# Kernel optimization log

Measured on AMD Instinct MI355X. Metric: run time of the kernel, lower is better.

The kernel has to match this reference:

```python
import jax, jax.numpy as jnp
import numpy as np

B, N, D, H, DG = 1, 1024, 512, 8, 64
DK = D // H
EPS = 1e-5


def _layer_norm(x, g, b):
    m = jnp.mean(x, axis=-1, keepdims=True)
    v = jnp.var(x, axis=-1, keepdims=True)
    return (x - m) / jnp.sqrt(v + EPS) * g + b


def _box_rel_embedding(box):
    # box: (B, N, 4) = x_min, y_min, x_max, y_max
    x_min, y_min, x_max, y_max = [box[..., i] for i in range(4)]  # each (B, N)
    cx = (x_min + x_max) * 0.5
    cy = (y_min + y_max) * 0.5
    w = x_max - x_min + 1.0
    h = y_max - y_min + 1.0
    dx = jnp.log(jnp.clip(jnp.abs((cx[:, :, None] - cx[:, None, :]) / w[:, :, None]), 0.001))
    dy = jnp.log(jnp.clip(jnp.abs((cy[:, :, None] - cy[:, None, :]) / h[:, :, None]), 0.001))
    dw = jnp.log(w[:, :, None] / w[:, None, :])
    dh = jnp.log(h[:, :, None] / h[:, None, :])
    pos = jnp.stack([dx, dy, dw, dh], axis=-1)  # (B, N, N, 4)
    dim_mat = 1.0 / jnp.power(1000.0, jnp.arange(DG // 8, dtype=jnp.float32) / (DG // 8))  # (8,)
    mul = (100.0 * pos[..., None] * dim_mat).reshape(pos.shape[0], pos.shape[1], pos.shape[2], -1)  # (B,N,N,32)
    return jnp.concatenate([jnp.sin(mul), jnp.cos(mul)], axis=-1)  # (B, N, N, 64)


def _split_heads(x, W, b):
    # torch permute(2,0,1,3).view(-1, len, d_k): head-major flattening
    return (x @ W.T + b).reshape(B, N, H, DK).transpose(2, 0, 1, 3).reshape(H * B, N, DK)


def _forward(input_query, input_key, input_value, input_box,
             Wq, bq, Wk, bk, Wv, bv, Wo, bo, WG_w, WG_b,
             ln0_g, ln0_b, ln_g, ln_b):
    residual = input_query
    emb = _box_rel_embedding(input_box)  # (B, N, N, 64)
    # per-head linear (64 -> 1) then relu: (B, H, N, N)
    w_g = jax.nn.relu(jnp.einsum('bijg,hg->bhij', emb, WG_w) + WG_b[None, :, None, None])
    q = _split_heads(input_query, Wq, bq)  # (H*B, N, DK)
    k = _split_heads(input_key, Wk, bk)
    v = _split_heads(input_value, Wv, bv)
    scores = jnp.einsum('xnd,xmd->xnm', q, k) / np.sqrt(DK).astype(np.float32)  # (H*B, N, N)
    # original adds (B,H,N,N) to (H*B,N,N): only valid for B==1
    w_mn = jax.nn.softmax(jnp.log(jnp.clip(w_g.reshape(H * B, N, N), 1e-6)) + scores, axis=-1)
    x = jnp.einsum('xnm,xmd->xnd', w_mn, v)  # (H*B, N, DK)
    # faithful to original: transpose(1,2) then view(nbatches, -1, h*d_k)
    x = x.transpose(0, 2, 1).reshape(B, -1, H * DK)  # (B, N, D)
    out0 = _layer_norm(x + residual, ln0_g, ln0_b)
    out = out0 @ Wo.T + bo  # dropout = identity (eval mode)
    return _layer_norm(out + out0, ln_g, ln_b)


def setup_inputs() -> dict:
    key = jax.random.key(0)
    ks = jax.random.split(key, 12)
    inp = {}
    inp['input_query'] = jax.random.normal(ks[0], (B, N, D), dtype=jnp.float32)
    inp['input_key'] = jax.random.normal(ks[1], (B, N, D), dtype=jnp.float32)
    inp['input_value'] = jax.random.normal(ks[2], (B, N, D), dtype=jnp.float32)
    mins = jax.random.uniform(ks[3], (B, N, 2), dtype=jnp.float32) * 500.0
    sizes = jax.random.uniform(ks[4], (B, N, 2), dtype=jnp.float32) * 99.0 + 1.0
    inp['input_box'] = jnp.concatenate([mins, mins + sizes], axis=-1)  # valid boxes
    s = 0.02
    inp['Wq'] = jax.random.normal(ks[5], (D, D), dtype=jnp.float32) * s
    inp['bq'] = jnp.zeros((D,), dtype=jnp.float32)
    inp['Wk'] = jax.random.normal(ks[6], (D, D), dtype=jnp.float32) * s
    inp['bk'] = jnp.zeros((D,), dtype=jnp.float32)
    inp['Wv'] = jax.random.normal(ks[7], (D, D), dtype=jnp.float32) * s
    inp['bv'] = jnp.zeros((D,), dtype=jnp.float32)
    inp['Wo'] = jax.random.normal(ks[8], (D, D), dtype=jnp.float32) * s
    inp['bo'] = jnp.zeros((D,), dtype=jnp.float32)
    inp['WG_w'] = jax.random.normal(ks[9], (H, DG), dtype=jnp.float32) * 0.1
    inp['WG_b'] = jax.random.normal(ks[10], (H,), dtype=jnp.float32) * 0.1
    inp['ln0_g'] = jnp.ones((D,), dtype=jnp.float32)
    inp['ln0_b'] = jnp.zeros((D,), dtype=jnp.float32)
    inp['ln_g'] = jnp.ones((D,), dtype=jnp.float32)
    inp['ln_b'] = jnp.zeros((D,), dtype=jnp.float32)
    return inp


def reference(input_query, input_key, input_value, input_box,
              Wq, bq, Wk, bk, Wv, bv, Wo, bo, WG_w, WG_b,
              ln0_g, ln0_b, ln_g, ln_b):
    return _forward(input_query, input_key, input_value, input_box,
                    Wq, bq, Wk, bk, Wv, bv, Wo, bo, WG_w, WG_b,
                    ln0_g, ln0_b, ln_g, ln_b)
```

## Files before the change

### kernel.cpp

```cpp
#include <hip/hip_runtime.h>
#include <cstddef>

#define NTOK 1024
#define DMODEL 512
#define NHEAD 8
#define DKH 64
#define NSPLIT 4
#define JQ 256

typedef __attribute__((ext_vector_type(4))) float f32x4;
typedef __attribute__((ext_vector_type(8))) __bf16 bf16x8;
typedef __attribute__((ext_vector_type(4))) __bf16 bf16x4;
typedef __attribute__((ext_vector_type(4))) unsigned short u16x4;
typedef __attribute__((ext_vector_type(8))) unsigned short u16x8;
typedef __attribute__((ext_vector_type(4))) _Float16 f16x4;
typedef unsigned short ushort_t;

__device__ __forceinline__ float wave_sum_f(float v){
  #pragma unroll
  for (int m=1; m<64; m<<=1) v += __shfl_xor(v, m, 64);
  return v;
}
__device__ __forceinline__ unsigned short f2bf(float f){
  __bf16 b = (__bf16)f;
  return __builtin_bit_cast(unsigned short, b);
}
__device__ __forceinline__ float bf2f(unsigned short u){
  return (float)__builtin_bit_cast(__bf16, u);
}

__device__ __forceinline__ float fract_hw(float x){
  float r; asm("v_fract_f32 %0, %1" : "=v"(r) : "v"(x)); return r;
}
__device__ __forceinline__ float sin_rev(float rev){
  float f = fract_hw(rev);
  float s; asm("v_sin_f32 %0, %1" : "=v"(s) : "v"(f)); return s;
}
__device__ __forceinline__ float cos_rev(float rev){
  float f = fract_hw(rev);
  float c; asm("v_cos_f32 %0, %1" : "=v"(c) : "v"(f)); return c;
}
__device__ __forceinline__ float log_hw(float x){
  float l; asm("v_log_f32 %0, %1" : "=v"(l) : "v"(x));
  return 0.69314718056f * l;
}
__device__ __forceinline__ float exp_hw(float x){
  float y = x * 1.44269504f;
  float e; asm("v_exp_f32 %0, %1" : "=v"(e) : "v"(y));
  return e;
}

__global__ __launch_bounds__(256) void k_pre(
    const float* __restrict__ box, const float* __restrict__ WGw, const float* __restrict__ WGb,
    _Float16* __restrict__ wg16,
    const float* __restrict__ q, const float* __restrict__ k, const float* __restrict__ v,
    const float* __restrict__ wq, const float* __restrict__ wk, const float* __restrict__ wv,
    const float* __restrict__ wo,
    ushort_t* __restrict__ qb, ushort_t* __restrict__ kb, ushort_t* __restrict__ vb,
    ushort_t* __restrict__ wqb, ushort_t* __restrict__ wkb, ushort_t* __restrict__ wvb,
    ushort_t* __restrict__ wob){
  const int t = threadIdx.x;
  if (blockIdx.x >= 1024){
    int gi = (blockIdx.x - 1024)*256 + t;
    const float* s; ushort_t* d; int off;
    if (gi < 196608){
      int seg = gi >> 16;
      off = (gi & 65535)*8;
      s = seg==0 ? q : seg==1 ? k : v;
      d = seg==0 ? qb : seg==1 ? kb : vb;
    } else {
      int g2 = gi - 196608;
      int seg = g2 >> 15;
      off = (g2 & 32767)*8;
      s = seg==0 ? wq : seg==1 ? wk : seg==2 ? wv : wo;
      d = seg==0 ? wqb : seg==1 ? wkb : seg==2 ? wvb : wob;
    }
    float4 a = *(const float4*)(s + off);
    float4 b = *(const float4*)(s + off + 4);
    u16x4 o0, o1;
    o0[0]=f2bf(a.x); o0[1]=f2bf(a.y); o0[2]=f2bf(a.z); o0[3]=f2bf(a.w);
    o1[0]=f2bf(b.x); o1[1]=f2bf(b.y); o1[2]=f2bf(b.z); o1[3]=f2bf(b.w);
    *(u16x4*)(d + off) = o0;
    *(u16x4*)(d + off + 4) = o1;
    return;
  }
  __shared__ float arr[4][1024];
  #pragma unroll
  for (int u=0; u<4; u++){
    int idx = u*256 + t;
    float4 b4 = *(const float4*)(box + idx*4);
    arr[0][idx] = (b4.x + b4.z)*0.5f;
    arr[1][idx] = (b4.y + b4.w)*0.5f;
    arr[2][idx] = log_hw(b4.z - b4.x + 1.0f);
    arr[3][idx] = log_hw(b4.w - b4.y + 1.0f);
  }
  const int i = blockIdx.x;
  const int lane = t & 63, w = t >> 6, li = lane & 15, g = lane >> 4;
  float4 bi = *(const float4*)(box + i*4);
  float wi = bi.z - bi.x + 1.0f, hi = bi.w - bi.y + 1.0f;
  float Pi = (g==0) ? (bi.x+bi.z)*0.5f : (g==1) ? (bi.y+bi.w)*0.5f
           : (g==2) ? log_hw(wi) : log_hw(hi);
  float Ri = (g==0) ? 1.0f/wi : (g==1) ? 1.0f/hi : 1.0f;
  const bool doLog = (g < 2);
  bf16x8 wfs = {}, wfc = {};
  float wgb_li = 0.0f;
  if (li < 8){
    #pragma unroll
    for (int e=0; e<8; e++){
      wfs[e] = (__bf16)WGw[li*64 + g*8 + e];
      wfc[e] = (__bf16)WGw[li*64 + 32 + g*8 + e];
    }
    wgb_li = WGb[li];
  }
  __syncthreads();
  const float* parr = &arr[g][0];
  const float DMrev[8] = {15.9154943f, 6.7115094f, 2.8302196f, 1.1934938f,
                          0.5032921f, 0.2122365f, 0.08949941f, 0.0377416f};
  const int jbeg = w*256;
  for (int it=0; it<16; ++it){
    int j = jbeg + it*16 + li;
    float diff = (Pi - parr[j])*Ri;
    float lg = log_hw(fmaxf(fabsf(diff), 1e-3f));
    float dv = doLog ? lg : diff;
    bf16x8 afs, afc;
    #pragma unroll
    for (int e=0; e<8; e++){
      float rev = dv * DMrev[e];
      afs[e] = (__bf16)sin_rev(rev);
      afc[e] = (__bf16)cos_rev(rev);
    }
    f32x4 acc = (f32x4){0.f,0.f,0.f,0.f};
    acc = __builtin_amdgcn_mfma_f32_16x16x32_bf16(afs, wfs, acc, 0,0,0);
    acc = __builtin_amdgcn_mfma_f32_16x16x32_bf16(afc, wfc, acc, 0,0,0);
    if (li < 8){
      f16x4 o;
      #pragma unroll
      for (int r=0; r<4; r++)
        o[r] = (_Float16)fmaxf(acc[r] + wgb_li, 6.103515625e-05f);
      *(f16x4*)(wg16 + (((size_t)li<<20) + ((size_t)i<<10) + jbeg + it*16 + g*4)) = o;
    }
  }
}

__global__ __launch_bounds__(128) void k_mm_qkv(
    const ushort_t* __restrict__ Aq, const ushort_t* __restrict__ Ak, const ushort_t* __restrict__ Av,
    const ushort_t* __restrict__ Wqb, const ushort_t* __restrict__ Wkb, const ushort_t* __restrict__ Wvb,
    const float* __restrict__ bq, const float* __restrict__ bk, const float* __restrict__ bv,
    ushort_t* __restrict__ Qb, ushort_t* __restrict__ Kb, ushort_t* __restrict__ Vt){
  const int z = blockIdx.z;
  const ushort_t* A = z==0 ? Aq : z==1 ? Ak : Av;
  const ushort_t* W = z==0 ? Wqb : z==1 ? Wkb : Wvb;
  const float* bias = z==0 ? bq : z==1 ? bk : bv;
  const int t = threadIdx.x, lane = t & 63, w = t >> 6;
  const int li = lane & 15, g = lane >> 4;
  const int m0 = blockIdx.y*32;
  const int n0 = blockIdx.x*64 + w*32;
  const ushort_t* ar = A + (size_t)(m0+li)*DMODEL + g*8;
  const ushort_t* wr = W + (size_t)(n0+li)*DMODEL + g*8;
  f32x4 acc[2][2] = {};
  if (z < 2){
    #pragma unroll
    for (int k0=0; k0<DMODEL; k0+=64){
      bf16x8 wf0a = *(const bf16x8*)(wr + k0);
      bf16x8 wf0b = *(const bf16x8*)(wr + k0 + 32);
      bf16x8 wf1a = *(const bf16x8*)(wr + 16*DMODEL + k0);
      bf16x8 wf1b = *(const bf16x8*)(wr + 16*DMODEL + k0 + 32);
      bf16x8 af0a = *(const bf16x8*)(ar + k0);
      bf16x8 af0b = *(const bf16x8*)(ar + k0 + 32);
      bf16x8 af1a = *(const bf16x8*)(ar + 16*DMODEL + k0);
      bf16x8 af1b = *(const bf16x8*)(ar + 16*DMODEL + k0 + 32);
      acc[0][0] = __builtin_amdgcn_mfma_f32_16x16x32_bf16(wf0a, af0a, acc[0][0], 0,0,0);
      acc[0][0] = __builtin_amdgcn_mfma_f32_16x16x32_bf16(wf0b, af0b, acc[0][0], 0,0,0);
      acc[0][1] = __builtin_amdgcn_mfma_f32_16x16x32_bf16(wf0a, af1a, acc[0][1], 0,0,0);
      acc[0][1] = __builtin_amdgcn_mfma_f32_16x16x32_bf16(wf0b, af1b, acc[0][1], 0,0,0);
      acc[1][0] = __builtin_amdgcn_mfma_f32_16x16x32_bf16(wf1a, af0a, acc[1][0], 0,0,0);
      acc[1][0] = __builtin_amdgcn_mfma_f32_16x16x32_bf16(wf1b, af0b, acc[1][0], 0,0,0);
      acc[1][1] = __builtin_amdgcn_mfma_f32_16x16x32_bf16(wf1a, af1a, acc[1][1], 0,0,0);
      acc[1][1] = __builtin_amdgcn_mfma_f32_16x16x32_bf16(wf1b, af1b, acc[1][1], 0,0,0);
    }
    ushort_t* C = z ? Kb : Qb;
    #pragma unroll
    for (int nf=0; nf<2; nf++){
      int n = n0 + nf*16 + g*4;
      float4 b4 = *(const float4*)(bias + n);
      const float* bp = (const float*)&b4;
      #pragma unroll
      for (int mf=0; mf<2; mf++){
        int m = m0 + mf*16 + li;
        u16x4 o;
        #pragma unroll
        for (int r=0; r<4; r++) o[r] = f2bf(acc[nf][mf][r] + bp[r]);
        *(u16x4*)(C + (size_t)m*DMODEL + n) = o;
      }
    }
  } else {
    #pragma unroll
    for (int k0=0; k0<DMODEL; k0+=64){
      bf16x8 wf0a = *(const bf16x8*)(wr + k0);
      bf16x8 wf0b = *(const bf16x8*)(wr + k0 + 32);
      bf16x8 wf1a = *(const bf16x8*)(wr + 16*DMODEL + k0);
      bf16x8 wf1b = *(const bf16x8*)(wr + 16*DMODEL + k0 + 32);
      bf16x8 af0a = *(const bf16x8*)(ar + k0);
      bf16x8 af0b = *(const bf16x8*)(ar + k0 + 32);
      bf16x8 af1a = *(const bf16x8*)(ar + 16*DMODEL + k0);
      bf16x8 af1b = *(const bf16x8*)(ar + 16*DMODEL + k0 + 32);
      acc[0][0] = __builtin_amdgcn_mfma_f32_16x16x32_bf16(af0a, wf0a, acc[0][0], 0,0,0);
      acc[0][0] = __builtin_amdgcn_mfma_f32_16x16x32_bf16(af0b, wf0b, acc[0][0], 0,0,0);
      acc[0][1] = __builtin_amdgcn_mfma_f32_16x16x32_bf16(af0a, wf1a, acc[0][1], 0,0,0);
      acc[0][1] = __builtin_amdgcn_mfma_f32_16x16x32_bf16(af0b, wf1b, acc[0][1], 0,0,0);
      acc[1][0] = __builtin_amdgcn_mfma_f32_16x16x32_bf16(af1a, wf0a, acc[1][0], 0,0,0);
      acc[1][0] = __builtin_amdgcn_mfma_f32_16x16x32_bf16(af1b, wf0b, acc[1][0], 0,0,0);
      acc[1][1] = __builtin_amdgcn_mfma_f32_16x16x32_bf16(af1a, wf1a, acc[1][1], 0,0,0);
      acc[1][1] = __builtin_amdgcn_mfma_f32_16x16x32_bf16(af1b, wf1b, acc[1][1], 0,0,0);
    }
    #pragma unroll
    for (int mf=0; mf<2; mf++){
      int m = m0 + mf*16 + g*4;
      #pragma unroll
      for (int nf=0; nf<2; nf++){
        int n = n0 + nf*16 + li;
        float bn = bias[n];
        u16x4 o;
        #pragma unroll
        for (int r=0; r<4; r++) o[r] = f2bf(acc[mf][nf][r] + bn);
        *(u16x4*)(Vt + (((size_t)(n>>6))<<16) + ((size_t)(n&63)<<10) + m) = o;
      }
    }
  }
}

__global__ __launch_bounds__(512) void k_attn3(const ushort_t* __restrict__ Qb,
     const ushort_t* __restrict__ Kb, const ushort_t* __restrict__ Vt,
     const _Float16* __restrict__ wg, ushort_t* __restrict__ Xpt, float* __restrict__ rsp){
  __shared__ ushort_t Ks[256*68];
  __shared__ ushort_t Vs[64*264];
  const int t = threadIdx.x;
  const int itg = blockIdx.x, h = blockIdx.y, sp = blockIdx.z;
  const int jbeg = sp*JQ;
  {
    const int r = t >> 3, c = (t & 7)*8;
    #pragma unroll
    for (int p=0; p<4; p++){
      u16x8 kv = *(const u16x8*)(Kb + (size_t)(jbeg + p*64 + r)*DMODEL + h*DKH + c);
      *(u16x8*)(Ks + (p*64 + r)*68 + c) = kv;
      u16x8 vv = *(const u16x8*)(Vt + ((size_t)h<<16) + (size_t)r*NTOK + jbeg + p*64 + c);
      *(u16x8*)(Vs + r*264 + p*64 + c) = vv;
    }
  }
  const int lane = t & 63, w = t >> 6;
  const int i0 = (itg*8 + w)*16;
  const int li = lane & 15, g = lane >> 4;
  const ushort_t* qp = Qb + (size_t)(i0+li)*DMODEL + h*DKH + g*8;
  bf16x8 qf0 = *(const bf16x8*)(qp);
  bf16x8 qf1 = *(const bf16x8*)(qp + 32);
  const _Float16* gbase = wg + ((size_t)h<<20) + ((size_t)(i0+li)<<10) + jbeg + g*4;
  f32x4 xacc[4];
  #pragma unroll
  for (int mf=0; mf<4; mf++) xacc[mf] = (f32x4){0.f,0.f,0.f,0.f};
  float rsum = 0.f;
  __syncthreads();
  #pragma unroll
  for (int jj = 0; jj < JQ; jj += 32){
    const ushort_t* kp = Ks + (jj + li)*68 + g*8;
    bf16x8 a00 = *(const bf16x8*)(kp);
    bf16x8 a01 = *(const bf16x8*)(kp + 32);
    bf16x8 a10 = *(const bf16x8*)(kp + 16*68);
    bf16x8 a11 = *(const bf16x8*)(kp + 16*68 + 32);
    f32x4 s0 = (f32x4){0.f,0.f,0.f,0.f};
    f32x4 s1 = (f32x4){0.f,0.f,0.f,0.f};
    s0 = __builtin_amdgcn_mfma_f32_16x16x32_bf16(a00, qf0, s0, 0,0,0);
    s0 = __builtin_amdgcn_mfma_f32_16x16x32_bf16(a01, qf1, s0, 0,0,0);
    s1 = __builtin_amdgcn_mfma_f32_16x16x32_bf16(a10, qf0, s1, 0,0,0);
    s1 = __builtin_amdgcn_mfma_f32_16x16x32_bf16(a11, qf1, s1, 0,0,0);
    f16x4 g0 = *(const f16x4*)(gbase + jj);
    f16x4 g1 = *(const f16x4*)(gbase + jj + 16);
    float p[8];
    #pragma unroll
    for (int r=0; r<4; r++){ p[r]   = (float)g0[r] * exp_hw(s0[r]*0.125f); rsum += p[r]; }
    #pragma unroll
    for (int r=0; r<4; r++){ p[4+r] = (float)g1[r] * exp_hw(s1[r]*0.125f); rsum += p[4+r]; }
    bf16x8 pb;
    pb[0]=(__bf16)p[0]; pb[1]=(__bf16)p[1]; pb[2]=(__bf16)p[2]; pb[3]=(__bf16)p[3];
    pb[4]=(__bf16)p[4]; pb[5]=(__bf16)p[5]; pb[6]=(__bf16)p[6]; pb[7]=(__bf16)p[7];
    #pragma unroll
    for (int mf=0; mf<4; mf++){
      const ushort_t* vp = Vs + (size_t)(li + mf*16)*264 + jj + g*4;
      bf16x4 lo = *(const bf16x4*)(vp);
      bf16x4 hi = *(const bf16x4*)(vp + 16);
      bf16x8 vf = __builtin_shufflevector(lo, hi, 0,1,2,3,4,5,6,7);
      xacc[mf] = __builtin_amdgcn_mfma_f32_16x16x32_bf16(vf, pb, xacc[mf], 0,0,0);
    }
  }
  rsum += __shfl_xor(rsum, 16, 64);
  rsum += __shfl_xor(rsum, 32, 64);
  if (lane < 16) rsp[((size_t)sp*NHEAD + h)*NTOK + i0 + li] = rsum;
  __syncthreads();
  float* xw = (float*)Ks + w*(16*68);
  #pragma unroll
  for (int mf=0; mf<4; mf++)
    *(f32x4*)&xw[li*68 + mf*16 + g*4] = xacc[mf];
  __builtin_amdgcn_s_waitcnt(0);
  float xv[16];
  #pragma unroll
  for (int r=0; r<16; r++) xv[r] = xw[r*68 + lane];
  u16x8 o0, o1;
  #pragma unroll
  for (int r=0; r<8; r++){ o0[r] = f2bf(xv[r]); o1[r] = f2bf(xv[8+r]); }
  ushort_t* xp = Xpt + (((size_t)sp*NHEAD + h)*DKH + lane)*NTOK + i0;
  *(u16x8*)(xp)     = o0;
  *(u16x8*)(xp + 8) = o1;
}

__global__ __launch_bounds__(256) void k_ln0c(const ushort_t* __restrict__ Xpt,
        const float* __restrict__ rsp, const float* __restrict__ resid,
        const float* __restrict__ g, const float* __restrict__ b,
        float* __restrict__ out0, ushort_t* __restrict__ out0b){
  const int n = blockIdx.x, t = threadIdx.x;
  const int h = n >> 7, dk = (n >> 1) & 63, mo = (n & 1)*512;
  const int i0 = mo + t, i1 = mo + t + 256;
  float s0v=0.f, s1v=0.f, r0=0.f, r1=0.f;
  #pragma unroll
  for (int sp=0; sp<NSPLIT; sp++){
    const ushort_t* base = Xpt + (((size_t)sp*NHEAD + h)*DKH + dk)*NTOK;
    s0v += bf2f(base[i0]);
    s1v += bf2f(base[i1]);
    const float* rb = rsp + ((size_t)sp*NHEAD + h)*NTOK;
    r0 += rb[i0];
    r1 += rb[i1];
  }
  float x0 = s0v/r0 + resid[(size_t)n*DMODEL + t];
  float x1 = s1v/r1 + resid[(size_t)n*DMODEL + t + 256];
  __shared__ float red[8];
  float s = wave_sum_f(x0 + x1);
  float q = wave_sum_f(x0*x0 + x1*x1);
  int wid = t >> 6, lane = t & 63;
  if (lane == 0){ red[wid] = s; red[4+wid] = q; }
  __syncthreads();
  float S = red[0]+red[1]+red[2]+red[3];
  float Q = red[4]+red[5]+red[6]+red[7];
  float mean = S * (1.0f/512.0f);
  float var = Q * (1.0f/512.0f) - mean*mean;
  float rs = rsqrtf(var + 1e-5f);
  float y0 = (x0-mean)*rs*g[t] + b[t];
  float y1 = (x1-mean)*rs*g[t+256] + b[t+256];
  out0[(size_t)n*DMODEL + t]        = y0;
  out0[(size_t)n*DMODEL + t + 256]  = y1;
  out0b[(size_t)n*DMODEL + t]       = f2bf(y0);
  out0b[(size_t)n*DMODEL + t + 256] = f2bf(y1);
}

__global__ __launch_bounds__(512) void k_mm_o_ln(
    const ushort_t* __restrict__ A, const ushort_t* __restrict__ W,
    const float* __restrict__ bo, const float* __restrict__ add,
    const float* __restrict__ lng, const float* __restrict__ lnb, float* __restrict__ out){
  const int t = threadIdx.x, lane = t & 63, w = t >> 6;
  const int li = lane & 15, g = lane >> 4;
  const int m0 = blockIdx.x*16;
  const int n0 = w*64;
  const ushort_t* ar = A + (size_t)(m0+li)*DMODEL + g*8;
  const ushort_t* wr = W + (size_t)(n0+li)*DMODEL + g*8;
  f32x4 acc[4] = {};
  #pragma unroll
  for (int k0=0; k0<DMODEL; k0+=64){
    bf16x8 afa = *(const bf16x8*)(ar + k0);
    bf16x8 afb = *(const bf16x8*)(ar + k0 + 32);
    #pragma unroll
    for (int nf=0; nf<4; nf++){
      const ushort_t* wp = wr + (size_t)nf*16*DMODEL + k0;
      bf16x8 wfa = *(const bf16x8*)(wp);
      bf16x8 wfb = *(const bf16x8*)(wp + 32);
      acc[nf] = __builtin_amdgcn_mfma_f32_16x16x32_bf16(wfa, afa, acc[nf], 0,0,0);
      acc[nf] = __builtin_amdgcn_mfma_f32_16x16x32_bf16(wfb, afb, acc[nf], 0,0,0);
    }
  }
  const int m = m0 + li;
  float s = 0.f, qq = 0.f;
  f32x4 v[4];
  #pragma unroll
  for (int nf=0; nf<4; nf++){
    int n = n0 + nf*16 + g*4;
    f32x4 b4 = *(const f32x4*)(bo + n);
    f32x4 a4 = *(const f32x4*)(add + (size_t)m*DMODEL + n);
    #pragma unroll
    for (int r=0; r<4; r++){
      float x = acc[nf][r] + b4[r] + a4[r];
      v[nf][r] = x; s += x; qq += x*x;
    }
  }
  s  += __shfl_xor(s, 16, 64);  s  += __shfl_xor(s, 32, 64);
  qq += __shfl_xor(qq, 16, 64); qq += __shfl_xor(qq, 32, 64);
  __shared__ float red[8][16][2];
  if (g == 0){ red[w][li][0] = s; red[w][li][1] = qq; }
  __syncthreads();
  float S = 0.f, Q = 0.f;
  #pragma unroll
  for (int u=0; u<8; u++){ S += red[u][li][0]; Q += red[u][li][1]; }
  float mean = S * (1.0f/512.0f);
  float var = Q * (1.0f/512.0f) - mean*mean;
  float rs = rsqrtf(var + 1e-5f);
  #pragma unroll
  for (int nf=0; nf<4; nf++){
    int n = n0 + nf*16 + g*4;
    f32x4 g4 = *(const f32x4*)(lng + n);
    f32x4 be = *(const f32x4*)(lnb + n);
    f32x4 o;
    #pragma unroll
    for (int r=0; r<4; r++) o[r] = (v[nf][r]-mean)*rs*g4[r] + be[r];
    *(f32x4*)(out + (size_t)m*DMODEL + n) = o;
  }
}

extern "C" void kernel_launch(void* const* d_in, const int* in_sizes, int n_in,
                              void* d_out, int out_size, void* d_ws, size_t ws_size,
                              hipStream_t stream){
  (void)in_sizes; (void)n_in; (void)out_size; (void)ws_size;
  const float* in_q = (const float*)d_in[0];
  const float* in_k = (const float*)d_in[1];
  const float* in_v = (const float*)d_in[2];
  const float* box  = (const float*)d_in[3];
  const float* Wq   = (const float*)d_in[4];
  const float* bq   = (const float*)d_in[5];
  const float* Wk   = (const float*)d_in[6];
  const float* bk   = (const float*)d_in[7];
  const float* Wv   = (const float*)d_in[8];
  const float* bv   = (const float*)d_in[9];
  const float* Wo   = (const float*)d_in[10];
  const float* bo   = (const float*)d_in[11];
  const float* WGw  = (const float*)d_in[12];
  const float* WGb  = (const float*)d_in[13];
  const float* ln0g = (const float*)d_in[14];
  const float* ln0b = (const float*)d_in[15];
  const float* lng  = (const float*)d_in[16];
  const float* lnb  = (const float*)d_in[17];

  float* ws = (float*)d_ws;
  ushort_t* Abq  = (ushort_t*)(ws + 0);
  ushort_t* Abk  = (ushort_t*)(ws + 262144);
  ushort_t* Abv  = (ushort_t*)(ws + 524288);
  ushort_t* Wqb  = (ushort_t*)(ws + 786432);
  ushort_t* Wkb  = (ushort_t*)(ws + 917504);
  ushort_t* Wvb  = (ushort_t*)(ws + 1048576);
  ushort_t* Wob  = (ushort_t*)(ws + 1179648);
  ushort_t* Qb   = (ushort_t*)(ws + 1310720);
  ushort_t* Kb   = (ushort_t*)(ws + 1572864);
  ushort_t* Vt   = (ushort_t*)(ws + 1835008);
  _Float16* wg16 = (_Float16*)(ws + 2097152);
  ushort_t* Xpt  = (ushort_t*)(ws + 6291456);
  float*    rsp  = ws + 8388608;
  float*    out0 = ws + 8421376;
  ushort_t* out0b= (ushort_t*)(ws + 8945664);
  float*    out  = (float*)d_out;

  k_pre<<<dim3(2304), dim3(256), 0, stream>>>(box, WGw, WGb, wg16,
            in_q, in_k, in_v, Wq, Wk, Wv, Wo,
            Abq, Abk, Abv, Wqb, Wkb, Wvb, Wob);
  k_mm_qkv<<<dim3(8,32,3), dim3(128), 0, stream>>>(Abq, Abk, Abv, Wqb, Wkb, Wvb,
            bq, bk, bv, Qb, Kb, Vt);
  k_attn3<<<dim3(8,8,4), dim3(512), 0, stream>>>(Qb, Kb, Vt, wg16, Xpt, rsp);
  k_ln0c<<<dim3(1024), dim3(256), 0, stream>>>(Xpt, rsp, in_q, ln0g, ln0b, out0, out0b);
  k_mm_o_ln<<<dim3(64), dim3(512), 0, stream>>>(out0b, Wob, bo, out0, lng, lnb, out);
}
```

Measured before the change: 77.92 us.

## Fuse QKV projection into box-embedding kernel and LN0 into output GEMM

The QKV projection now reads fp32 inputs and weights directly, converts them to bf16 in registers, and runs as extra blocks of the box-embedding kernel. This removes the separate bf16 conversion pass and one launch. The LN0 combine step is fused into the output-projection+LN kernel through shared memory, which drops the out0/out0b round trip and another launch. In exchange, the QKV blocks now read fp32 data at twice the bytes and redo the conversion per tile, and the back kernel runs only 64 blocks that also do the LN0 work.

```diff
diff --git a/kernel.cpp b/kernel.cpp
--- a/kernel.cpp
+++ b/kernel.cpp
@@ -9,6 +9,7 @@
 #define JQ 256
 
 typedef __attribute__((ext_vector_type(4))) float f32x4;
+typedef __attribute__((ext_vector_type(8))) float f32x8;
 typedef __attribute__((ext_vector_type(8))) __bf16 bf16x8;
 typedef __attribute__((ext_vector_type(4))) __bf16 bf16x4;
 typedef __attribute__((ext_vector_type(4))) unsigned short u16x4;
@@ -28,6 +29,10 @@
 __device__ __forceinline__ float bf2f(unsigned short u){
   return (float)__builtin_bit_cast(__bf16, u);
 }
+__device__ __forceinline__ bf16x8 cvt8(const float* p){
+  f32x8 v = *(const f32x8*)p;
+  return __builtin_convertvector(v, bf16x8);
+}
 
 __device__ __forceinline__ float fract_hw(float x){
   float r; asm("v_fract_f32 %0, %1" : "=v"(r) : "v"(x)); return r;
@@ -50,38 +55,112 @@
   return e;
 }
 
-__global__ __launch_bounds__(256) void k_pre(
+__global__ __launch_bounds__(256) void k_front(
     const float* __restrict__ box, const float* __restrict__ WGw, const float* __restrict__ WGb,
     _Float16* __restrict__ wg16,
-    const float* __restrict__ q, const float* __restrict__ k, const float* __restrict__ v,
-    const float* __restrict__ wq, const float* __restrict__ wk, const float* __restrict__ wv,
-    const float* __restrict__ wo,
-    ushort_t* __restrict__ qb, ushort_t* __restrict__ kb, ushort_t* __restrict__ vb,
-    ushort_t* __restrict__ wqb, ushort_t* __restrict__ wkb, ushort_t* __restrict__ wvb,
-    ushort_t* __restrict__ wob){
+    const float* __restrict__ inq, const float* __restrict__ ink, const float* __restrict__ inv,
+    const float* __restrict__ Wq, const float* __restrict__ Wk, const float* __restrict__ Wv,
+    const float* __restrict__ Wo,
+    const float* __restrict__ bq, const float* __restrict__ bk, const float* __restrict__ bv,
+    ushort_t* __restrict__ Qb, ushort_t* __restrict__ Kb, ushort_t* __restrict__ Vt,
+    ushort_t* __restrict__ Wob){
   const int t = threadIdx.x;
-  if (blockIdx.x >= 1024){
-    int gi = (blockIdx.x - 1024)*256 + t;
-    const float* s; ushort_t* d; int off;
-    if (gi < 196608){
-      int seg = gi >> 16;
-      off = (gi & 65535)*8;
-      s = seg==0 ? q : seg==1 ? k : v;
-      d = seg==0 ? qb : seg==1 ? kb : vb;
-    } else {
-      int g2 = gi - 196608;
-      int seg = g2 >> 15;
-      off = (g2 & 32767)*8;
-      s = seg==0 ? wq : seg==1 ? wk : seg==2 ? wv : wo;
-      d = seg==0 ? wqb : seg==1 ? wkb : seg==2 ? wvb : wob;
-    }
-    float4 a = *(const float4*)(s + off);
-    float4 b = *(const float4*)(s + off + 4);
+  const int lane = t & 63, w = t >> 6, li = lane & 15, g = lane >> 4;
+  if (blockIdx.x >= 1408){
+    int gi = (blockIdx.x - 1408)*256 + t;
+    int off = gi*8;
+    float4 a = *(const float4*)(Wo + off);
+    float4 b4 = *(const float4*)(Wo + off + 4);
     u16x4 o0, o1;
     o0[0]=f2bf(a.x); o0[1]=f2bf(a.y); o0[2]=f2bf(a.z); o0[3]=f2bf(a.w);
-    o1[0]=f2bf(b.x); o1[1]=f2bf(b.y); o1[2]=f2bf(b.z); o1[3]=f2bf(b.w);
-    *(u16x4*)(d + off) = o0;
-    *(u16x4*)(d + off + 4) = o1;
+    o1[0]=f2bf(b4.x); o1[1]=f2bf(b4.y); o1[2]=f2bf(b4.z); o1[3]=f2bf(b4.w);
+    *(u16x4*)(Wob + off) = o0;
+    *(u16x4*)(Wob + off + 4) = o1;
+    return;
+  }
+  if (blockIdx.x >= 1024){
+    const int unit = (blockIdx.x - 1024)*2 + (w >> 1);
+    const int z = unit >> 8;
+    const int rem = unit & 255;
+    const int my = rem >> 3;
+    const int nx = rem & 7;
+    const int m0 = my*32;
+    const int n0 = nx*64 + (w & 1)*32;
+    const float* A = z==0 ? inq : z==1 ? ink : inv;
+    const float* W = z==0 ? Wq : z==1 ? Wk : Wv;
+    const float* bias = z==0 ? bq : z==1 ? bk : bv;
+    const float* ar = A + (size_t)(m0+li)*DMODEL + g*8;
+    const float* wr = W + (size_t)(n0+li)*DMODEL + g*8;
+    f32x4 acc[2][2] = {};
+    if (z < 2){
+      #pragma unroll
+      for (int k0=0; k0<DMODEL; k0+=64){
+        bf16x8 wf0a = cvt8(wr + k0);
+        bf16x8 wf0b = cvt8(wr + k0 + 32);
+        bf16x8 wf1a = cvt8(wr + 16*DMODEL + k0);
+        bf16x8 wf1b = cvt8(wr + 16*DMODEL + k0 + 32);
+        bf16x8 af0a = cvt8(ar + k0);
+        bf16x8 af0b = cvt8(ar + k0 + 32);
+        bf16x8 af1a = cvt8(ar + 16*DMODEL + k0);
+        bf16x8 af1b = cvt8(ar + 16*DMODEL + k0 + 32);
+        acc[0][0] = __builtin_amdgcn_mfma_f32_16x16x32_bf16(wf0a, af0a, acc[0][0], 0,0,0);
+        acc[0][0] = __builtin_amdgcn_mfma_f32_16x16x32_bf16(wf0b, af0b, acc[0][0], 0,0,0);
+        acc[0][1] = __builtin_amdgcn_mfma_f32_16x16x32_bf16(wf0a, af1a, acc[0][1], 0,0,0);
+        acc[0][1] = __builtin_amdgcn_mfma_f32_16x16x32_bf16(wf0b, af1b, acc[0][1], 0,0,0);
+        acc[1][0] = __builtin_amdgcn_mfma_f32_16x16x32_bf16(wf1a, af0a, acc[1][0], 0,0,0);
+        acc[1][0] = __builtin_amdgcn_mfma_f32_16x16x32_bf16(wf1b, af0b, acc[1][0], 0,0,0);
+        acc[1][1] = __builtin_amdgcn_mfma_f32_16x16x32_bf16(wf1a, af1a, acc[1][1], 0,0,0);
+        acc[1][1] = __builtin_amdgcn_mfma_f32_16x16x32_bf16(wf1b, af1b, acc[1][1], 0,0,0);
+      }
+      ushort_t* C = z ? Kb : Qb;
+      #pragma unroll
+      for (int nf=0; nf<2; nf++){
+        int n = n0 + nf*16 + g*4;
+        float4 b4 = *(const float4*)(bias + n);
+        const float* bp = (const float*)&b4;
+        #pragma unroll
+        for (int mf=0; mf<2; mf++){
+          int m = m0 + mf*16 + li;
+          u16x4 o;
+          #pragma unroll
+          for (int r=0; r<4; r++) o[r] = f2bf(acc[nf][mf][r] + bp[r]);
+          *(u16x4*)(C + (size_t)m*DMODEL + n) = o;
+        }
+      }
+    } else {
+      #pragma unroll
+      for (int k0=0; k0<DMODEL; k0+=64){
+        bf16x8 wf0a = cvt8(wr + k0);
+        bf16x8 wf0b = cvt8(wr + k0 + 32);
+        bf16x8 wf1a = cvt8(wr + 16*DMODEL + k0);
+        bf16x8 wf1b = cvt8(wr + 16*DMODEL + k0 + 32);
+        bf16x8 af0a = cvt8(ar + k0);
+        bf16x8 af0b = cvt8(ar + k0 + 32);
+        bf16x8 af1a = cvt8(ar + 16*DMODEL + k0);
+        bf16x8 af1b = cvt8(ar + 16*DMODEL + k0 + 32);
+        acc[0][0] = __builtin_amdgcn_mfma_f32_16x16x32_bf16(af0a, wf0a, acc[0][0], 0,0,0);
+        acc[0][0] = __builtin_amdgcn_mfma_f32_16x16x32_bf16(af0b, wf0b, acc[0][0], 0,0,0);
+        acc[0][1] = __builtin_amdgcn_mfma_f32_16x16x32_bf16(af0a, wf1a, acc[0][1], 0,0,0);
+        acc[0][1] = __builtin_amdgcn_mfma_f32_16x16x32_bf16(af0b, wf1b, acc[0][1], 0,0,0);
+        acc[1][0] = __builtin_amdgcn_mfma_f32_16x16x32_bf16(af1a, wf0a, acc[1][0], 0,0,0);
+        acc[1][0] = __builtin_amdgcn_mfma_f32_16x16x32_bf16(af1b, wf0b, acc[1][0], 0,0,0);
+        acc[1][1] = __builtin_amdgcn_mfma_f32_16x16x32_bf16(af1a, wf1a, acc[1][1], 0,0,0);
+        acc[1][1] = __builtin_amdgcn_mfma_f32_16x16x32_bf16(af1b, wf1b, acc[1][1], 0,0,0);
+      }
+      #pragma unroll
+      for (int mf=0; mf<2; mf++){
+        int m = m0 + mf*16 + g*4;
+        #pragma unroll
+        for (int nf=0; nf<2; nf++){
+          int n = n0 + nf*16 + li;
+          float bn = bias[n];
+          u16x4 o;
+          #pragma unroll
+          for (int r=0; r<4; r++) o[r] = f2bf(acc[mf][nf][r] + bn);
+          *(u16x4*)(Vt + (((size_t)(n>>6))<<16) + ((size_t)(n&63)<<10) + m) = o;
+        }
+      }
+    }
     return;
   }
   __shared__ float arr[4][1024];
@@ -95,7 +174,6 @@
     arr[3][idx] = log_hw(b4.w - b4.y + 1.0f);
   }
   const int i = blockIdx.x;
-  const int lane = t & 63, w = t >> 6, li = lane & 15, g = lane >> 4;
   float4 bi = *(const float4*)(box + i*4);
   float wi = bi.z - bi.x + 1.0f, hi = bi.w - bi.y + 1.0f;
   float Pi = (g==0) ? (bi.x+bi.z)*0.5f : (g==1) ? (bi.y+bi.w)*0.5f
@@ -138,93 +216,6 @@
       for (int r=0; r<4; r++)
         o[r] = (_Float16)fmaxf(acc[r] + wgb_li, 6.103515625e-05f);
       *(f16x4*)(wg16 + (((size_t)li<<20) + ((size_t)i<<10) + jbeg + it*16 + g*4)) = o;
-    }
-  }
-}
-
-__global__ __launch_bounds__(128) void k_mm_qkv(
-    const ushort_t* __restrict__ Aq, const ushort_t* __restrict__ Ak, const ushort_t* __restrict__ Av,
-    const ushort_t* __restrict__ Wqb, const ushort_t* __restrict__ Wkb, const ushort_t* __restrict__ Wvb,
-    const float* __restrict__ bq, const float* __restrict__ bk, const float* __restrict__ bv,
-    ushort_t* __restrict__ Qb, ushort_t* __restrict__ Kb, ushort_t* __restrict__ Vt){
-  const int z = blockIdx.z;
-  const ushort_t* A = z==0 ? Aq : z==1 ? Ak : Av;
-  const ushort_t* W = z==0 ? Wqb : z==1 ? Wkb : Wvb;
-  const float* bias = z==0 ? bq : z==1 ? bk : bv;
-  const int t = threadIdx.x, lane = t & 63, w = t >> 6;
-  const int li = lane & 15, g = lane >> 4;
-  const int m0 = blockIdx.y*32;
-  const int n0 = blockIdx.x*64 + w*32;
-  const ushort_t* ar = A + (size_t)(m0+li)*DMODEL + g*8;
-  const ushort_t* wr = W + (size_t)(n0+li)*DMODEL + g*8;
-  f32x4 acc[2][2] = {};
-  if (z < 2){
-    #pragma unroll
-    for (int k0=0; k0<DMODEL; k0+=64){
-      bf16x8 wf0a = *(const bf16x8*)(wr + k0);
-      bf16x8 wf0b = *(const bf16x8*)(wr + k0 + 32);
-      bf16x8 wf1a = *(const bf16x8*)(wr + 16*DMODEL + k0);
-      bf16x8 wf1b = *(const bf16x8*)(wr + 16*DMODEL + k0 + 32);
-      bf16x8 af0a = *(const bf16x8*)(ar + k0);
-      bf16x8 af0b = *(const bf16x8*)(ar + k0 + 32);
-      bf16x8 af1a = *(const bf16x8*)(ar + 16*DMODEL + k0);
-      bf16x8 af1b = *(const bf16x8*)(ar + 16*DMODEL + k0 + 32);
-      acc[0][0] = __builtin_amdgcn_mfma_f32_16x16x32_bf16(wf0a, af0a, acc[0][0], 0,0,0);
-      acc[0][0] = __builtin_amdgcn_mfma_f32_16x16x32_bf16(wf0b, af0b, acc[0][0], 0,0,0);
-      acc[0][1] = __builtin_amdgcn_mfma_f32_16x16x32_bf16(wf0a, af1a, acc[0][1], 0,0,0);
-      acc[0][1] = __builtin_amdgcn_mfma_f32_16x16x32_bf16(wf0b, af1b, acc[0][1], 0,0,0);
-      acc[1][0] = __builtin_amdgcn_mfma_f32_16x16x32_bf16(wf1a, af0a, acc[1][0], 0,0,0);
-      acc[1][0] = __builtin_amdgcn_mfma_f32_16x16x32_bf16(wf1b, af0b, acc[1][0], 0,0,0);
-      acc[1][1] = __builtin_amdgcn_mfma_f32_16x16x32_bf16(wf1a, af1a, acc[1][1], 0,0,0);
-      acc[1][1] = __builtin_amdgcn_mfma_f32_16x16x32_bf16(wf1b, af1b, acc[1][1], 0,0,0);
-    }
-    ushort_t* C = z ? Kb : Qb;
-    #pragma unroll
-    for (int nf=0; nf<2; nf++){
-      int n = n0 + nf*16 + g*4;
-      float4 b4 = *(const float4*)(bias + n);
-      const float* bp = (const float*)&b4;
-      #pragma unroll
-      for (int mf=0; mf<2; mf++){
-        int m = m0 + mf*16 + li;
-        u16x4 o;
-        #pragma unroll
-        for (int r=0; r<4; r++) o[r] = f2bf(acc[nf][mf][r] + bp[r]);
-        *(u16x4*)(C + (size_t)m*DMODEL + n) = o;
-      }
-    }
-  } else {
-    #pragma unroll
-    for (int k0=0; k0<DMODEL; k0+=64){
-      bf16x8 wf0a = *(const bf16x8*)(wr + k0);
-      bf16x8 wf0b = *(const bf16x8*)(wr + k0 + 32);
-      bf16x8 wf1a = *(const bf16x8*)(wr + 16*DMODEL + k0);
-      bf16x8 wf1b = *(const bf16x8*)(wr + 16*DMODEL + k0 + 32);
-      bf16x8 af0a = *(const bf16x8*)(ar + k0);
-      bf16x8 af0b = *(const bf16x8*)(ar + k0 + 32);
-      bf16x8 af1a = *(const bf16x8*)(ar + 16*DMODEL + k0);
-      bf16x8 af1b = *(const bf16x8*)(ar + 16*DMODEL + k0 + 32);
-      acc[0][0] = __builtin_amdgcn_mfma_f32_16x16x32_bf16(af0a, wf0a, acc[0][0], 0,0,0);
-      acc[0][0] = __builtin_amdgcn_mfma_f32_16x16x32_bf16(af0b, wf0b, acc[0][0], 0,0,0);
-      acc[0][1] = __builtin_amdgcn_mfma_f32_16x16x32_bf16(af0a, wf1a, acc[0][1], 0,0,0);
-      acc[0][1] = __builtin_amdgcn_mfma_f32_16x16x32_bf16(af0b, wf1b, acc[0][1], 0,0,0);
-      acc[1][0] = __builtin_amdgcn_mfma_f32_16x16x32_bf16(af1a, wf0a, acc[1][0], 0,0,0);
-      acc[1][0] = __builtin_amdgcn_mfma_f32_16x16x32_bf16(af1b, wf0b, acc[1][0], 0,0,0);
-      acc[1][1] = __builtin_amdgcn_mfma_f32_16x16x32_bf16(af1a, wf1a, acc[1][1], 0,0,0);
-      acc[1][1] = __builtin_amdgcn_mfma_f32_16x16x32_bf16(af1b, wf1b, acc[1][1], 0,0,0);
-    }
-    #pragma unroll
-    for (int mf=0; mf<2; mf++){
-      int m = m0 + mf*16 + g*4;
-      #pragma unroll
-      for (int nf=0; nf<2; nf++){
-        int n = n0 + nf*16 + li;
-        float bn = bias[n];
-        u16x4 o;
-        #pragma unroll
-        for (int r=0; r<4; r++) o[r] = f2bf(acc[mf][nf][r] + bn);
-        *(u16x4*)(Vt + (((size_t)(n>>6))<<16) + ((size_t)(n&63)<<10) + m) = o;
-      }
     }
   }
 }
@@ -311,54 +302,56 @@
   *(u16x8*)(xp + 8) = o1;
 }
 
-__global__ __launch_bounds__(256) void k_ln0c(const ushort_t* __restrict__ Xpt,
-        const float* __restrict__ rsp, const float* __restrict__ resid,
-        const float* __restrict__ g, const float* __restrict__ b,
-        float* __restrict__ out0, ushort_t* __restrict__ out0b){
-  const int n = blockIdx.x, t = threadIdx.x;
-  const int h = n >> 7, dk = (n >> 1) & 63, mo = (n & 1)*512;
-  const int i0 = mo + t, i1 = mo + t + 256;
-  float s0v=0.f, s1v=0.f, r0=0.f, r1=0.f;
-  #pragma unroll
-  for (int sp=0; sp<NSPLIT; sp++){
-    const ushort_t* base = Xpt + (((size_t)sp*NHEAD + h)*DKH + dk)*NTOK;
-    s0v += bf2f(base[i0]);
-    s1v += bf2f(base[i1]);
-    const float* rb = rsp + ((size_t)sp*NHEAD + h)*NTOK;
-    r0 += rb[i0];
-    r1 += rb[i1];
-  }
-  float x0 = s0v/r0 + resid[(size_t)n*DMODEL + t];
-  float x1 = s1v/r1 + resid[(size_t)n*DMODEL + t + 256];
-  __shared__ float red[8];
-  float s = wave_sum_f(x0 + x1);
-  float q = wave_sum_f(x0*x0 + x1*x1);
-  int wid = t >> 6, lane = t & 63;
-  if (lane == 0){ red[wid] = s; red[4+wid] = q; }
-  __syncthreads();
-  float S = red[0]+red[1]+red[2]+red[3];
-  float Q = red[4]+red[5]+red[6]+red[7];
-  float mean = S * (1.0f/512.0f);
-  float var = Q * (1.0f/512.0f) - mean*mean;
-  float rs = rsqrtf(var + 1e-5f);
-  float y0 = (x0-mean)*rs*g[t] + b[t];
-  float y1 = (x1-mean)*rs*g[t+256] + b[t+256];
-  out0[(size_t)n*DMODEL + t]        = y0;
-  out0[(size_t)n*DMODEL + t + 256]  = y1;
-  out0b[(size_t)n*DMODEL + t]       = f2bf(y0);
-  out0b[(size_t)n*DMODEL + t + 256] = f2bf(y1);
-}
-
-__global__ __launch_bounds__(512) void k_mm_o_ln(
-    const ushort_t* __restrict__ A, const ushort_t* __restrict__ W,
-    const float* __restrict__ bo, const float* __restrict__ add,
-    const float* __restrict__ lng, const float* __restrict__ lnb, float* __restrict__ out){
+__global__ __launch_bounds__(512) void k_back(
+    const ushort_t* __restrict__ Xpt, const float* __restrict__ rsp,
+    const float* __restrict__ inq,
+    const float* __restrict__ ln0g, const float* __restrict__ ln0b,
+    const ushort_t* __restrict__ Wob, const float* __restrict__ bo,
+    const float* __restrict__ lng, const float* __restrict__ lnb,
+    float* __restrict__ out){
+  __shared__ ushort_t Ab[16][520];
+  __shared__ float    Y[16][516];
+  __shared__ float    red[8][16][2];
   const int t = threadIdx.x, lane = t & 63, w = t >> 6;
   const int li = lane & 15, g = lane >> 4;
   const int m0 = blockIdx.x*16;
+  #pragma unroll
+  for (int rr2=0; rr2<2; rr2++){
+    const int rr = w*2 + rr2;
+    const int n = m0 + rr;
+    const int h = n >> 7, dk = (n >> 1) & 63, mo = (n & 1)*512;
+    float x[8];
+    float sum = 0.f, sq = 0.f;
+    #pragma unroll
+    for (int c=0; c<8; c++){
+      int d = c*64 + lane;
+      int i = mo + d;
+      float sv = 0.f, rv = 0.f;
+      #pragma unroll
+      for (int sp=0; sp<NSPLIT; sp++){
+        sv += bf2f(Xpt[(((size_t)sp*NHEAD + h)*DKH + dk)*NTOK + i]);
+        rv += rsp[((size_t)sp*NHEAD + h)*NTOK + i];
+      }
+      x[c] = sv/rv + inq[(size_t)n*DMODEL + d];
+      sum += x[c]; sq += x[c]*x[c];
+    }
+    sum = wave_sum_f(sum);
+    sq  = wave_sum_f(sq);
+    float mean = sum * (1.0f/512.0f);
+    float var = sq * (1.0f/512.0f) - mean*mean;
+    float rs = rsqrtf(var + 1e-5f);
+    #pragma unroll
+    for (int c=0; c<8; c++){
+      int d = c*64 + lane;
+      float y = (x[c]-mean)*rs*ln0g[d] + ln0b[d];
+      Y[rr][d] = y;
+      Ab[rr][d] = f2bf(y);
+    }
+  }
+  __syncthreads();
   const int n0 = w*64;
-  const ushort_t* ar = A + (size_t)(m0+li)*DMODEL + g*8;
-  const ushort_t* wr = W + (size_t)(n0+li)*DMODEL + g*8;
+  const ushort_t* ar = &Ab[li][g*8];
+  const ushort_t* wr = Wob + (size_t)(n0+li)*DMODEL + g*8;
   f32x4 acc[4] = {};
   #pragma unroll
   for (int k0=0; k0<DMODEL; k0+=64){
@@ -380,16 +373,14 @@
   for (int nf=0; nf<4; nf++){
     int n = n0 + nf*16 + g*4;
     f32x4 b4 = *(const f32x4*)(bo + n);
-    f32x4 a4 = *(const f32x4*)(add + (size_t)m*DMODEL + n);
     #pragma unroll
     for (int r=0; r<4; r++){
-      float x = acc[nf][r] + b4[r] + a4[r];
+      float x = acc[nf][r] + b4[r] + Y[li][n + r];
       v[nf][r] = x; s += x; qq += x*x;
     }
   }
   s  += __shfl_xor(s, 16, 64);  s  += __shfl_xor(s, 32, 64);
   qq += __shfl_xor(qq, 16, 64); qq += __shfl_xor(qq, 32, 64);
-  __shared__ float red[8][16][2];
   if (g == 0){ red[w][li][0] = s; red[w][li][1] = qq; }
   __syncthreads();
   float S = 0.f, Q = 0.f;
@@ -434,29 +425,18 @@
   const float* lnb  = (const float*)d_in[17];
 
   float* ws = (float*)d_ws;
-  ushort_t* Abq  = (ushort_t*)(ws + 0);
-  ushort_t* Abk  = (ushort_t*)(ws + 262144);
-  ushort_t* Abv  = (ushort_t*)(ws + 524288);
-  ushort_t* Wqb  = (ushort_t*)(ws + 786432);
-  ushort_t* Wkb  = (ushort_t*)(ws + 917504);
-  ushort_t* Wvb  = (ushort_t*)(ws + 1048576);
-  ushort_t* Wob  = (ushort_t*)(ws + 1179648);
-  ushort_t* Qb   = (ushort_t*)(ws + 1310720);
-  ushort_t* Kb   = (ushort_t*)(ws + 1572864);
-  ushort_t* Vt   = (ushort_t*)(ws + 1835008);
-  _Float16* wg16 = (_Float16*)(ws + 2097152);
-  ushort_t* Xpt  = (ushort_t*)(ws + 6291456);
-  float*    rsp  = ws + 8388608;
-  float*    out0 = ws + 8421376;
-  ushort_t* out0b= (ushort_t*)(ws + 8945664);
+  ushort_t* Wob  = (ushort_t*)(ws + 0);
+  ushort_t* Qb   = (ushort_t*)(ws + 131072);
+  ushort_t* Kb   = (ushort_t*)(ws + 393216);
+  ushort_t* Vt   = (ushort_t*)(ws + 655360);
+  _Float16* wg16 = (_Float16*)(ws + 917504);
+  ushort_t* Xpt  = (ushort_t*)(ws + 5111808);
+  float*    rsp  = ws + 6160384;
   float*    out  = (float*)d_out;
 
-  k_pre<<<dim3(2304), dim3(256), 0, stream>>>(box, WGw, WGb, wg16,
-            in_q, in_k, in_v, Wq, Wk, Wv, Wo,
-            Abq, Abk, Abv, Wqb, Wkb, Wvb, Wob);
-  k_mm_qkv<<<dim3(8,32,3), dim3(128), 0, stream>>>(Abq, Abk, Abv, Wqb, Wkb, Wvb,
-            bq, bk, bv, Qb, Kb, Vt);
+  k_front<<<dim3(1536), dim3(256), 0, stream>>>(box, WGw, WGb, wg16,
+            in_q, in_k, in_v, Wq, Wk, Wv, Wo, bq, bk, bv, Qb, Kb, Vt, Wob);
   k_attn3<<<dim3(8,8,4), dim3(512), 0, stream>>>(Qb, Kb, Vt, wg16, Xpt, rsp);
-  k_ln0c<<<dim3(1024), dim3(256), 0, stream>>>(Xpt, rsp, in_q, ln0g, ln0b, out0, out0b);
-  k_mm_o_ln<<<dim3(64), dim3(512), 0, stream>>>(out0b, Wob, bo, out0, lng, lnb, out);
-}
+  k_back<<<dim3(64), dim3(512), 0, stream>>>(Xpt, rsp, in_q, ln0g, ln0b,
+            Wob, bo, lng, lnb, out);
+}
```

Result: slower. 83.15 us (+6.7%).

## Split attention keys eightfold and fuse split-reduce, LN0 and output projection

Applied to the files above, without the earlier changes.

The attention kernel now splits the key dimension into 8 chunks of 128 instead of 4 of 256, doubling the block count to 512 and halving per-block shared memory for better CU occupancy. The separate split-combine/LayerNorm kernel and the output-projection+LayerNorm kernel are merged into one kernel that reduces the partial sums, normalizes rows into shared memory, and feeds the MFMA projection directly. This removes one launch and the global round trip of the intermediate fp32 and bf16 activations. In exchange the reduction reads twice as many partial buffers and the fused kernel runs only 64 blocks, so the reduce phase has limited parallelism.

```diff
diff --git a/kernel.cpp b/kernel.cpp
--- a/kernel.cpp
+++ b/kernel.cpp
@@ -5,8 +5,8 @@
 #define DMODEL 512
 #define NHEAD 8
 #define DKH 64
-#define NSPLIT 4
-#define JQ 256
+#define NSPLIT 8
+#define JQ 128
 
 typedef __attribute__((ext_vector_type(4))) float f32x4;
 typedef __attribute__((ext_vector_type(8))) __bf16 bf16x8;
@@ -229,22 +229,23 @@
   }
 }
 
-__global__ __launch_bounds__(512) void k_attn3(const ushort_t* __restrict__ Qb,
+__global__ __launch_bounds__(512) void k_attn4(const ushort_t* __restrict__ Qb,
      const ushort_t* __restrict__ Kb, const ushort_t* __restrict__ Vt,
      const _Float16* __restrict__ wg, ushort_t* __restrict__ Xpt, float* __restrict__ rsp){
-  __shared__ ushort_t Ks[256*68];
-  __shared__ ushort_t Vs[64*264];
+  __shared__ __align__(16) char smem[34816];
+  ushort_t* Ks = (ushort_t*)smem;
+  ushort_t* Vs = (ushort_t*)(smem + 17408);
   const int t = threadIdx.x;
   const int itg = blockIdx.x, h = blockIdx.y, sp = blockIdx.z;
   const int jbeg = sp*JQ;
   {
     const int r = t >> 3, c = (t & 7)*8;
     #pragma unroll
-    for (int p=0; p<4; p++){
+    for (int p=0; p<2; p++){
       u16x8 kv = *(const u16x8*)(Kb + (size_t)(jbeg + p*64 + r)*DMODEL + h*DKH + c);
       *(u16x8*)(Ks + (p*64 + r)*68 + c) = kv;
       u16x8 vv = *(const u16x8*)(Vt + ((size_t)h<<16) + (size_t)r*NTOK + jbeg + p*64 + c);
-      *(u16x8*)(Vs + r*264 + p*64 + c) = vv;
+      *(u16x8*)(Vs + r*136 + p*64 + c) = vv;
     }
   }
   const int lane = t & 63, w = t >> 6;
@@ -284,7 +285,7 @@
     pb[4]=(__bf16)p[4]; pb[5]=(__bf16)p[5]; pb[6]=(__bf16)p[6]; pb[7]=(__bf16)p[7];
     #pragma unroll
     for (int mf=0; mf<4; mf++){
-      const ushort_t* vp = Vs + (size_t)(li + mf*16)*264 + jj + g*4;
+      const ushort_t* vp = Vs + (size_t)(li + mf*16)*136 + jj + g*4;
       bf16x4 lo = *(const bf16x4*)(vp);
       bf16x4 hi = *(const bf16x4*)(vp + 16);
       bf16x8 vf = __builtin_shufflevector(lo, hi, 0,1,2,3,4,5,6,7);
@@ -295,7 +296,7 @@
   rsum += __shfl_xor(rsum, 32, 64);
   if (lane < 16) rsp[((size_t)sp*NHEAD + h)*NTOK + i0 + li] = rsum;
   __syncthreads();
-  float* xw = (float*)Ks + w*(16*68);
+  float* xw = (float*)smem + w*(16*68);
   #pragma unroll
   for (int mf=0; mf<4; mf++)
     *(f32x4*)&xw[li*68 + mf*16 + g*4] = xacc[mf];
@@ -311,54 +312,56 @@
   *(u16x8*)(xp + 8) = o1;
 }
 
-__global__ __launch_bounds__(256) void k_ln0c(const ushort_t* __restrict__ Xpt,
-        const float* __restrict__ rsp, const float* __restrict__ resid,
-        const float* __restrict__ g, const float* __restrict__ b,
-        float* __restrict__ out0, ushort_t* __restrict__ out0b){
-  const int n = blockIdx.x, t = threadIdx.x;
-  const int h = n >> 7, dk = (n >> 1) & 63, mo = (n & 1)*512;
-  const int i0 = mo + t, i1 = mo + t + 256;
-  float s0v=0.f, s1v=0.f, r0=0.f, r1=0.f;
-  #pragma unroll
-  for (int sp=0; sp<NSPLIT; sp++){
-    const ushort_t* base = Xpt + (((size_t)sp*NHEAD + h)*DKH + dk)*NTOK;
-    s0v += bf2f(base[i0]);
-    s1v += bf2f(base[i1]);
-    const float* rb = rsp + ((size_t)sp*NHEAD + h)*NTOK;
-    r0 += rb[i0];
-    r1 += rb[i1];
-  }
-  float x0 = s0v/r0 + resid[(size_t)n*DMODEL + t];
-  float x1 = s1v/r1 + resid[(size_t)n*DMODEL + t + 256];
-  __shared__ float red[8];
-  float s = wave_sum_f(x0 + x1);
-  float q = wave_sum_f(x0*x0 + x1*x1);
-  int wid = t >> 6, lane = t & 63;
-  if (lane == 0){ red[wid] = s; red[4+wid] = q; }
-  __syncthreads();
-  float S = red[0]+red[1]+red[2]+red[3];
-  float Q = red[4]+red[5]+red[6]+red[7];
-  float mean = S * (1.0f/512.0f);
-  float var = Q * (1.0f/512.0f) - mean*mean;
-  float rs = rsqrtf(var + 1e-5f);
-  float y0 = (x0-mean)*rs*g[t] + b[t];
-  float y1 = (x1-mean)*rs*g[t+256] + b[t+256];
-  out0[(size_t)n*DMODEL + t]        = y0;
-  out0[(size_t)n*DMODEL + t + 256]  = y1;
-  out0b[(size_t)n*DMODEL + t]       = f2bf(y0);
-  out0b[(size_t)n*DMODEL + t + 256] = f2bf(y1);
-}
-
-__global__ __launch_bounds__(512) void k_mm_o_ln(
-    const ushort_t* __restrict__ A, const ushort_t* __restrict__ W,
-    const float* __restrict__ bo, const float* __restrict__ add,
-    const float* __restrict__ lng, const float* __restrict__ lnb, float* __restrict__ out){
+__global__ __launch_bounds__(512) void k_back(
+    const ushort_t* __restrict__ Xpt, const float* __restrict__ rsp,
+    const float* __restrict__ inq,
+    const float* __restrict__ ln0g, const float* __restrict__ ln0b,
+    const ushort_t* __restrict__ Wob, const float* __restrict__ bo,
+    const float* __restrict__ lng, const float* __restrict__ lnb,
+    float* __restrict__ out){
+  __shared__ ushort_t Ab[16][520];
+  __shared__ float    Y[16][516];
+  __shared__ float    red[8][16][2];
   const int t = threadIdx.x, lane = t & 63, w = t >> 6;
   const int li = lane & 15, g = lane >> 4;
   const int m0 = blockIdx.x*16;
+  #pragma unroll
+  for (int rr2=0; rr2<2; rr2++){
+    const int rr = w*2 + rr2;
+    const int n = m0 + rr;
+    const int h = n >> 7, dk = (n >> 1) & 63, mo = (n & 1)*512;
+    float x[8];
+    float sum = 0.f, sq = 0.f;
+    #pragma unroll
+    for (int c=0; c<8; c++){
+      int d = c*64 + lane;
+      int i = mo + d;
+      float sv = 0.f, rv = 0.f;
+      #pragma unroll
+      for (int sp=0; sp<NSPLIT; sp++){
+        sv += bf2f(Xpt[(((size_t)sp*NHEAD + h)*DKH + dk)*NTOK + i]);
+        rv += rsp[((size_t)sp*NHEAD + h)*NTOK + i];
+      }
+      x[c] = sv/rv + inq[(size_t)n*DMODEL + d];
+      sum += x[c]; sq += x[c]*x[c];
+    }
+    sum = wave_sum_f(sum);
+    sq  = wave_sum_f(sq);
+    float mean = sum * (1.0f/512.0f);
+    float var = sq * (1.0f/512.0f) - mean*mean;
+    float rs = rsqrtf(var + 1e-5f);
+    #pragma unroll
+    for (int c=0; c<8; c++){
+      int d = c*64 + lane;
+      float y = (x[c]-mean)*rs*ln0g[d] + ln0b[d];
+      Y[rr][d] = y;
+      Ab[rr][d] = f2bf(y);
+    }
+  }
+  __syncthreads();
   const int n0 = w*64;
-  const ushort_t* ar = A + (size_t)(m0+li)*DMODEL + g*8;
-  const ushort_t* wr = W + (size_t)(n0+li)*DMODEL + g*8;
+  const ushort_t* ar = &Ab[li][g*8];
+  const ushort_t* wr = Wob + (size_t)(n0+li)*DMODEL + g*8;
   f32x4 acc[4] = {};
   #pragma unroll
   for (int k0=0; k0<DMODEL; k0+=64){
@@ -380,16 +383,14 @@
   for (int nf=0; nf<4; nf++){
     int n = n0 + nf*16 + g*4;
     f32x4 b4 = *(const f32x4*)(bo + n);
-    f32x4 a4 = *(const f32x4*)(add + (size_t)m*DMODEL + n);
     #pragma unroll
     for (int r=0; r<4; r++){
-      float x = acc[nf][r] + b4[r] + a4[r];
+      float x = acc[nf][r] + b4[r] + Y[li][n + r];
       v[nf][r] = x; s += x; qq += x*x;
     }
   }
   s  += __shfl_xor(s, 16, 64);  s  += __shfl_xor(s, 32, 64);
   qq += __shfl_xor(qq, 16, 64); qq += __shfl_xor(qq, 32, 64);
-  __shared__ float red[8][16][2];
   if (g == 0){ red[w][li][0] = s; red[w][li][1] = qq; }
   __syncthreads();
   float S = 0.f, Q = 0.f;
@@ -447,8 +448,6 @@
   _Float16* wg16 = (_Float16*)(ws + 2097152);
   ushort_t* Xpt  = (ushort_t*)(ws + 6291456);
   float*    rsp  = ws + 8388608;
-  float*    out0 = ws + 8421376;
-  ushort_t* out0b= (ushort_t*)(ws + 8945664);
   float*    out  = (float*)d_out;
 
   k_pre<<<dim3(2304), dim3(256), 0, stream>>>(box, WGw, WGb, wg16,
@@ -456,7 +455,7 @@
             Abq, Abk, Abv, Wqb, Wkb, Wvb, Wob);
   k_mm_qkv<<<dim3(8,32,3), dim3(128), 0, stream>>>(Abq, Abk, Abv, Wqb, Wkb, Wvb,
             bq, bk, bv, Qb, Kb, Vt);
-  k_attn3<<<dim3(8,8,4), dim3(512), 0, stream>>>(Qb, Kb, Vt, wg16, Xpt, rsp);
-  k_ln0c<<<dim3(1024), dim3(256), 0, stream>>>(Xpt, rsp, in_q, ln0g, ln0b, out0, out0b);
-  k_mm_o_ln<<<dim3(64), dim3(512), 0, stream>>>(out0b, Wob, bo, out0, lng, lnb, out);
-}
+  k_attn4<<<dim3(8,8,8), dim3(512), 0, stream>>>(Qb, Kb, Vt, wg16, Xpt, rsp);
+  k_back<<<dim3(64), dim3(512), 0, stream>>>(Xpt, rsp, in_q, ln0g, ln0b,
+            Wob, bo, lng, lnb, out);
+}
```

After: 88.91 us. 1.14x slower.
